# Optimization experiments

Measured on AMD Instinct MI355X. Metric: run time of the kernel, lower is better.

The kernel has to match this reference:

```python
import jax, jax.numpy as jnp
import numpy as np

LR_MEMORY = 0.01
CHUNK = 128


def _mlp(W0, b0, W1, b1, x):
    # linear -> SiLU -> linear (no activation on last layer)
    h = jax.nn.silu(x @ W0.T + b0)
    return h @ W1.T + b1


def setup_inputs() -> dict:
    key = jax.random.key(0)
    ks = jax.random.split(key, 8)
    B, L, D, M = 2, 2048, 2048, 2048
    x = jax.random.normal(ks[0], (B, L, D), jnp.float32)
    # kaiming_uniform (linear gain): bound = sqrt(3/fan_in); biases zero
    bw0 = float(np.sqrt(3.0 / D))
    bw1 = float(np.sqrt(3.0 / M))
    W0 = jax.random.uniform(ks[1], (M, D), jnp.float32, -bw0, bw0)
    b0 = jnp.zeros((M,), jnp.float32)
    W1 = jax.random.uniform(ks[2], (D, M), jnp.float32, -bw1, bw1)
    b1 = jnp.zeros((D,), jnp.float32)
    # lr_gate / forget_gate: nn.Linear(D,1) default init ~ U(-1/sqrt(D), 1/sqrt(D))
    bl = float(np.sqrt(1.0 / D))
    lr_w = jax.random.uniform(ks[3], (1, D), jnp.float32, -bl, bl)
    lr_b = jax.random.uniform(ks[4], (1,), jnp.float32, -bl, bl)
    fg_w = jax.random.uniform(ks[5], (1, D), jnp.float32, -bl, bl)
    fg_b = jax.random.uniform(ks[6], (1,), jnp.float32, -bl, bl)
    return {"x": x, "W0": W0, "b0": b0, "W1": W1, "b1": b1,
            "lr_w": lr_w, "lr_b": lr_b, "fg_w": fg_w, "fg_b": fg_b}


def reference(x, W0, b0, W1, b1, lr_w, lr_b, fg_w, fg_b):
    # Training-mode forward (create_graph=True path): gradients of the
    # chunk-wise fast-weight updates stay connected across chunks.
    B, L, D = x.shape
    C = min(CHUNK, L)
    n = L // C
    chunks = x.reshape(B, n, C, D).transpose(1, 0, 2, 3)  # (n, B, C, D)

    def loss_fn(params, chunk):
        pred = _mlp(*params, chunk)
        # target is detached in the torch code (chunk.detach())
        return jnp.mean((pred - jax.lax.stop_gradient(chunk)) ** 2)

    def step(params, chunk):
        grads = jax.grad(loss_fn)(params, chunk)
        eff_lr = LR_MEMORY * jnp.mean(jax.nn.sigmoid(chunk @ lr_w.T + lr_b))
        forget = jnp.mean(jax.nn.sigmoid(chunk.mean(axis=1) @ fg_w.T + fg_b))
        new_params = tuple(forget * p - eff_lr * g for p, g in zip(params, grads))
        out = _mlp(*new_params, chunk)  # re-forward through updated weights
        return new_params, out

    _, outs = jax.lax.scan(step, (W0, b0, W1, b1), chunks)  # outs: (n, B, C, D)
    return outs.transpose(1, 0, 2, 3).reshape(B, L, D)
```

## Files before the change

### kernel.cpp

```cpp
#include <hip/hip_runtime.h>
#include <hip/hip_bf16.h>
#include <cstddef>
#include <cstdint>

#define DD 2048
#define NRW 256
#define NCHUNK 16
#define CSZ 128
#define SCDP 4096.0f
#define NSTEP 16

typedef _Float16 h16;
typedef __attribute__((ext_vector_type(8))) _Float16 f16x8;
typedef __attribute__((ext_vector_type(4))) _Float16 f16x4;
typedef __attribute__((ext_vector_type(4))) float f32x4;

__device__ __forceinline__ float sigm(float v){ return 1.f/(1.f+__expf(-v)); }
__device__ __forceinline__ int xrow(int r, int t){ return (r>>7)*2048 + t*CSZ + (r&127); }
__device__ __forceinline__ f32x4 mfma16(f16x8 a, f16x8 b, f32x4 c){
  return __builtin_amdgcn_mfma_f32_16x16x32_f16(a, b, c, 0, 0, 0);
}

#define SBAR() do{ __builtin_amdgcn_sched_barrier(0); __builtin_amdgcn_s_barrier(); __builtin_amdgcn_sched_barrier(0); }while(0)
#define VMCNT(n) asm volatile("s_waitcnt vmcnt(" #n ")" ::: "memory")

__device__ __forceinline__ void gload16(const h16* g, h16* l){
  __builtin_amdgcn_global_load_lds((const __attribute__((address_space(1))) void*)g,
                                   (__attribute__((address_space(3))) void*)l, 16, 0, 0);
}

template<int MODE>
__global__ __launch_bounds__(512) void rowgemm(
    const h16* __restrict__ A, const h16* __restrict__ Bm,
    const float* __restrict__ bias,
    const float* __restrict__ x, int t,
    const h16* __restrict__ dsin, h16* __restrict__ dsout,
    float* __restrict__ ofp,
    h16* __restrict__ ob, h16* __restrict__ obT)
{
  __shared__ __align__(16) h16 As[3][32][128];
  __shared__ __align__(16) h16 Bs[3][64][128];
  __shared__ __align__(16) h16 Tb[64][36];
  const int tid = threadIdx.x;
  const int j0 = blockIdx.x * 64;
  const int r0 = blockIdx.y * 32;
  const int wid = tid >> 6, lane = tid & 63;
  const int wm = wid >> 2, wn = wid & 3;
  const int lr_ = lane & 15, lk = lane >> 4;
  const int sl4 = lane >> 4, su = lane & 15;
  const int arow = wid*4 + sl4;
  const int brow0 = wid*4 + sl4;
  const int brow1 = 32 + wid*4 + sl4;
  const size_t aoff  = (size_t)(r0 + arow)*DD + (size_t)((su ^ (arow&7))*8);
  const size_t boff0 = (size_t)(j0 + brow0)*DD + (size_t)((su ^ (brow0&7))*8);
  const size_t boff1 = (size_t)(j0 + brow1)*DD + (size_t)((su ^ (brow1&7))*8);
  h16* const as_base = &As[0][0][0];
  h16* const bs_base = &Bs[0][0][0];

  auto STAGE = [&](int b, int s){
    const size_t k0 = (size_t)s*128;
    gload16(A  + aoff  + k0, as_base + b*4096 + wid*512);
    gload16(Bm + boff0 + k0, bs_base + b*8192 + wid*512);
    gload16(Bm + boff1 + k0, bs_base + b*8192 + (wid+8)*512);
  };

  const int ar = wm*16 + lr_;
  const int br = wn*16 + lr_;
  int aidx[4], bidx[4];
#pragma unroll
  for (int q=0;q<4;++q){
    aidx[q] = ar*128 + ((q*4+lk)^(ar&7))*8;
    bidx[q] = br*128 + ((q*4+lk)^(br&7))*8;
  }

  f32x4 acc = {0.f,0.f,0.f,0.f};
  STAGE(0,0); STAGE(1,1);
  for (int s = 0; s < NSTEP; ++s){
    if (s < NSTEP-2){ STAGE((s+2)%3, s+2); VMCNT(6); }
    else if (s == NSTEP-2){ VMCNT(3); }
    else { VMCNT(0); }
    SBAR();
    const int cur = s%3;
    f16x8 a[4], b[4];
#pragma unroll
    for (int q=0;q<4;++q){
      a[q] = *(const f16x8*)(as_base + cur*4096 + aidx[q]);
      b[q] = *(const f16x8*)(bs_base + cur*8192 + bidx[q]);
    }
#pragma unroll
    for (int q=0;q<4;++q) acc = mfma16(a[q], b[q], acc);
    SBAR();
  }

  const int gc = j0 + wn*16 + lr_;
  const float bv = (MODE != 2) ? bias[gc] : 0.f;
#pragma unroll
  for (int ii=0;ii<4;++ii){
    const int gr = r0 + wm*16 + lk*4 + ii;
    float v = acc[ii] + bv;
    if (MODE == 0){
      float sg = sigm(v);
      float hval = v*sg;
      dsout[(size_t)gr*DD + gc] = (h16)(sg*(1.f + v*(1.f - sg)));
      ob[(size_t)gr*DD + gc] = (h16)hval;
      Tb[wn*16 + lr_][wm*16 + lk*4 + ii] = (h16)hval;
    } else if (MODE == 1){
      float xv = x[(size_t)xrow(gr,t)*DD + gc];
      float dpv = (SCDP*2.f/524288.f)*(v - xv);
      ob[(size_t)gr*DD + gc] = (h16)dpv;
      Tb[wn*16 + lr_][wm*16 + lk*4 + ii] = (h16)dpv;
    } else if (MODE == 2){
      float dzv = v * (float)dsin[(size_t)gr*DD + gc];
      Tb[wn*16 + lr_][wm*16 + lk*4 + ii] = (h16)dzv;
    } else if (MODE == 3){
      float sg = sigm(v);
      ob[(size_t)gr*DD + gc] = (h16)(v*sg);
    } else {
      ofp[(size_t)xrow(gr,t)*DD + gc] = v;
    }
  }
  if (MODE == 0 || MODE == 1 || MODE == 2){
    __syncthreads();
    const int lrow = tid >> 3, c4 = (tid & 7)*4;
    *(f16x4*)&obT[(size_t)(j0+lrow)*NRW + r0 + c4] = *(const f16x4*)&Tb[lrow][c4];
  }
}

template<int MODE>
__global__ __launch_bounds__(256) void gradup(
    const h16* __restrict__ A, const h16* __restrict__ Bm,
    h16* __restrict__ Wh, h16* __restrict__ WTh,
    const float* __restrict__ scal)
{
  __shared__ __align__(16) h16 As[2][64][128];
  __shared__ __align__(16) h16 Bs[2][64][128];
  __shared__ __align__(16) h16 Tb[64][72];
  const int tid = threadIdx.x;
  const int j0 = blockIdx.x * 64;
  const int i0 = blockIdx.y * 64;
  const int wid = tid >> 6, lane = tid & 63;
  const int wm = wid >> 1, wn = wid & 1;
  const int lr_ = lane & 15, lk = lane >> 4;
  const int sl4 = lane >> 4, su = lane & 15;
  h16* const as_base = &As[0][0][0];
  h16* const bs_base = &Bs[0][0][0];

#pragma unroll
  for (int h=0; h<2; ++h){
#pragma unroll
    for (int i=0;i<4;++i){
      const int c = wid*4 + i;
      const int row = c*4 + sl4;
      const size_t go = (size_t)row*NRW + (size_t)(h*128 + ((su ^ (row&7))*8));
      gload16(A  + (size_t)i0*NRW + go, as_base + h*8192 + c*512);
      gload16(Bm + (size_t)j0*NRW + go, bs_base + h*8192 + c*512);
    }
  }

  const int ra0 = wm*32 + lr_, ra1 = ra0 + 16;
  const int rb0 = wn*32 + lr_, rb1 = rb0 + 16;
  f32x4 acc[2][2] = {};
#pragma unroll
  for (int h=0; h<2; ++h){
    if (h==0){ VMCNT(8); } else { VMCNT(0); }
    SBAR();
#pragma unroll
    for (int ks=0; ks<4; ++ks){
      f16x8 a0 = *(const f16x8*)(as_base + h*8192 + ra0*128 + ((ks*4+lk)^(ra0&7))*8);
      f16x8 a1 = *(const f16x8*)(as_base + h*8192 + ra1*128 + ((ks*4+lk)^(ra1&7))*8);
      f16x8 b0 = *(const f16x8*)(bs_base + h*8192 + rb0*128 + ((ks*4+lk)^(rb0&7))*8);
      f16x8 b1 = *(const f16x8*)(bs_base + h*8192 + rb1*128 + ((ks*4+lk)^(rb1&7))*8);
      acc[0][0] = mfma16(a0,b0,acc[0][0]);
      acc[0][1] = mfma16(a0,b1,acc[0][1]);
      acc[1][0] = mfma16(a1,b0,acc[1][0]);
      acc[1][1] = mfma16(a1,b1,acc[1][1]);
    }
  }

  const float lrs = scal[0] * (1.f/SCDP);
  const float fg  = scal[1];
#pragma unroll
  for (int ri=0;ri<2;++ri)
#pragma unroll
  for (int cj=0;cj<2;++cj)
#pragma unroll
  for (int ii=0;ii<4;++ii){
    const int gi = i0 + wm*32 + ri*16 + lk*4 + ii;
    const int gj = j0 + wn*32 + cj*16 + lr_;
    const size_t idx = (size_t)gi*DD + gj;
    float wv = fg*(float)Wh[idx] - lrs*acc[ri][cj][ii];
    Wh[idx] = (h16)wv;
    if (MODE==0) Tb[wn*32+cj*16+lr_][wm*32+ri*16+lk*4+ii] = (h16)wv;
  }
  if (MODE==0){
    __syncthreads();
    const int lrow = tid >> 2, c16 = (tid & 3)*16;
    *(f16x8*)&WTh[(size_t)(j0+lrow)*DD + i0 + c16]   = *(const f16x8*)&Tb[lrow][c16];
    *(f16x8*)&WTh[(size_t)(j0+lrow)*DD + i0 + c16+8] = *(const f16x8*)&Tb[lrow][c16+8];
  }
}

__global__ __launch_bounds__(256) void xprep(const float* __restrict__ x, int t,
    const float* __restrict__ lr_w, const float* __restrict__ fg_w,
    h16* __restrict__ xh, h16* __restrict__ xT,
    float* __restrict__ rowacc, float* __restrict__ accs)
{
  __shared__ __align__(16) h16 Tb[64][72];
  __shared__ float red[4];
  const int tid = threadIdx.x;
  const int j0 = blockIdx.x*64, r0 = blockIdx.y*64;
  const int c4 = (tid & 15)*4, g = tid >> 4;
  const float4 lw = *(const float4*)&lr_w[j0+c4];
  const float4 fw = *(const float4*)&fg_w[j0+c4];
  float sfall = 0.f;
  float slv[4];
#pragma unroll
  for (int i=0;i<4;++i){
    const int row = g + i*16;
    float4 xv = *(const float4*)&x[(size_t)xrow(r0+row, t)*DD + j0 + c4];
    f16x4 hv; hv[0]=(h16)xv.x; hv[1]=(h16)xv.y; hv[2]=(h16)xv.z; hv[3]=(h16)xv.w;
    *(f16x4*)&xh[(size_t)(r0+row)*DD + j0 + c4] = hv;
    Tb[c4+0][row]=hv[0]; Tb[c4+1][row]=hv[1]; Tb[c4+2][row]=hv[2]; Tb[c4+3][row]=hv[3];
    float sl = xv.x*lw.x + xv.y*lw.y + xv.z*lw.z + xv.w*lw.w;
    float sf = xv.x*fw.x + xv.y*fw.y + xv.z*fw.z + xv.w*fw.w;
#pragma unroll
    for (int m=1;m<16;m<<=1) sl += __shfl_xor(sl, m);
    slv[i] = sl;
    sfall += sf;
  }
#pragma unroll
  for (int m=1;m<64;m<<=1) sfall += __shfl_xor(sfall, m);
  if ((tid&63)==0) red[tid>>6] = sfall;
  __syncthreads();
  if ((tid&15)==0){
#pragma unroll
    for (int i=0;i<4;++i) atomicAdd(&rowacc[r0 + g + i*16], slv[i]);
  }
  if (tid==0) atomicAdd(&accs[1 + (blockIdx.y>>1)], red[0]+red[1]+red[2]+red[3]);
  const int lcol = tid >> 2, r16 = (tid & 3)*16;
  *(f16x8*)&xT[(size_t)(j0+lcol)*NRW + r0 + r16]   = *(const f16x8*)&Tb[lcol][r16];
  *(f16x8*)&xT[(size_t)(j0+lcol)*NRW + r0 + r16+8] = *(const f16x8*)&Tb[lcol][r16+8];
}

__global__ __launch_bounds__(256) void finalize(
    float* __restrict__ rowacc, float* __restrict__ accs,
    const float* __restrict__ lr_b, const float* __restrict__ fg_b,
    float* __restrict__ scal)
{
  __shared__ float red[256];
  const int tid = threadIdx.x;
  float s = sigm(rowacc[tid] + lr_b[0]);
  rowacc[tid] = 0.f;
  red[tid] = s; __syncthreads();
  for (int o=128;o>0;o>>=1){ if (tid<o) red[tid]+=red[tid+o]; __syncthreads(); }
  if (tid==0){
    scal[0] = 0.01f * red[0] * (1.f/256.f);
    scal[1] = 0.5f*( sigm(accs[1]*(1.f/128.f) + fg_b[0]) + sigm(accs[2]*(1.f/128.f) + fg_b[0]) );
    accs[1] = 0.f; accs[2] = 0.f;
  }
}

__global__ __launch_bounds__(256) void bias_update(
    const h16* __restrict__ dpT, const h16* __restrict__ dzT,
    float* __restrict__ b1c, float* __restrict__ b0c,
    const float* __restrict__ scal)
{
  const int j = blockIdx.x*256 + threadIdx.x;
  const float lrs = scal[0] * (1.f/SCDP), fg = scal[1];
  const h16* src = (j < DD) ? &dpT[(size_t)j*NRW] : &dzT[(size_t)(j-DD)*NRW];
  float s = 0.f;
  const f16x8* p = (const f16x8*)src;
#pragma unroll 4
  for (int q = 0; q < 32; ++q){
    f16x8 v = p[q];
#pragma unroll
    for (int e = 0; e < 8; ++e) s += (float)v[e];
  }
  if (j < DD) b1c[j]    = fg*b1c[j]    - lrs*s;
  else        b0c[j-DD] = fg*b0c[j-DD] - lrs*s;
}

__global__ __launch_bounds__(256) void init_w1(const float* __restrict__ Wc,
    h16* __restrict__ Wh, h16* __restrict__ WTh)
{
  __shared__ __align__(16) h16 Tb[64][72];
  const int tid = threadIdx.x;
  const int j0 = blockIdx.x*64, i0 = blockIdx.y*64;
  const int c4 = (tid & 15)*4, rbase = tid >> 4;
#pragma unroll
  for (int i=0;i<4;++i){
    int row = rbase + i*16;
    float4 wv = *(const float4*)&Wc[(size_t)(i0+row)*DD + j0 + c4];
    f16x4 hv; hv[0]=(h16)wv.x; hv[1]=(h16)wv.y; hv[2]=(h16)wv.z; hv[3]=(h16)wv.w;
    *(f16x4*)&Wh[(size_t)(i0+row)*DD + j0 + c4] = hv;
    Tb[c4+0][row]=hv[0]; Tb[c4+1][row]=hv[1]; Tb[c4+2][row]=hv[2]; Tb[c4+3][row]=hv[3];
  }
  __syncthreads();
  const int lrow = tid >> 2, c16 = (tid & 3)*16;
  *(f16x8*)&WTh[(size_t)(j0+lrow)*DD + i0 + c16]   = *(const f16x8*)&Tb[lrow][c16];
  *(f16x8*)&WTh[(size_t)(j0+lrow)*DD + i0 + c16+8] = *(const f16x8*)&Tb[lrow][c16+8];
}

__global__ void init_w0(const float* __restrict__ Wc, h16* __restrict__ Wh){
  size_t i = ((size_t)blockIdx.x*256 + threadIdx.x)*4;
  float4 wv = *(const float4*)&Wc[i];
  f16x4 hv; hv[0]=(h16)wv.x; hv[1]=(h16)wv.y; hv[2]=(h16)wv.z; hv[3]=(h16)wv.w;
  *(f16x4*)&Wh[i] = hv;
}

extern "C" void kernel_launch(void* const* d_in, const int* in_sizes, int n_in,
                              void* d_out, int out_size, void* d_ws, size_t ws_size,
                              hipStream_t stream)
{
  const float* x    = (const float*)d_in[0];
  const float* W0   = (const float*)d_in[1];
  const float* b0   = (const float*)d_in[2];
  const float* W1   = (const float*)d_in[3];
  const float* b1   = (const float*)d_in[4];
  const float* lr_w = (const float*)d_in[5];
  const float* lr_b = (const float*)d_in[6];
  const float* fg_w = (const float*)d_in[7];
  const float* fg_b = (const float*)d_in[8];
  float* out = (float*)d_out;

  char* ws = (char*)d_ws;
  size_t off = 0;
  auto alloc = [&](size_t bytes)->char*{ char* p = ws + off; off += (bytes + 255) & ~255ull; return p; };
  float* b0c    = (float*)alloc(2048*4);
  float* b1c    = (float*)alloc(2048*4);
  float* stats  = (float*)alloc(1312);
  float* rowacc = stats;
  float* accs   = stats + 256;
  float* scal   = stats + 264;
  h16* W0h  = (h16*)alloc(4194304*2);
  h16* W1h  = (h16*)alloc(4194304*2);
  h16* W1Th = (h16*)alloc(4194304*2);
  h16* ds0h = (h16*)alloc(524288*2);
  h16* xh   = (h16*)alloc(524288*2);
  h16* xT   = (h16*)alloc(524288*2);
  h16* hb   = (h16*)alloc(524288*2);
  h16* hT   = (h16*)alloc(524288*2);
  h16* dpb  = (h16*)alloc(524288*2);
  h16* dpT  = (h16*)alloc(524288*2);
  h16* dzT  = (h16*)alloc(524288*2);
  h16* h2b  = (h16*)alloc(524288*2);

  hipMemcpyAsync(b0c, b0, 2048*sizeof(float), hipMemcpyDeviceToDevice, stream);
  hipMemcpyAsync(b1c, b1, 2048*sizeof(float), hipMemcpyDeviceToDevice, stream);
  hipMemsetAsync(stats, 0, 264*4, stream);

  dim3 blk256(256), blk512(512);
  init_w0<<<4096, blk256, 0, stream>>>(W0, W0h);
  init_w1<<<dim3(32,32), blk256, 0, stream>>>(W1, W1h, W1Th);

  for (int t = 0; t < NCHUNK; ++t){
    xprep<<<dim3(32,4), blk256, 0, stream>>>(x, t, lr_w, fg_w, xh, xT, rowacc, accs);
    finalize<<<1, blk256, 0, stream>>>(rowacc, accs, lr_b, fg_b, scal);
    rowgemm<0><<<dim3(32,8), blk512, 0, stream>>>(xh, W0h, b0c, nullptr, t, nullptr, ds0h, nullptr, hb, hT);
    rowgemm<1><<<dim3(32,8), blk512, 0, stream>>>(hb, W1h, b1c, x, t, nullptr, nullptr, nullptr, dpb, dpT);
    rowgemm<2><<<dim3(32,8), blk512, 0, stream>>>(dpb, W1Th, b1c, nullptr, t, ds0h, nullptr, nullptr, nullptr, dzT);
    gradup<0><<<dim3(32,32), blk256, 0, stream>>>(dpT, hT, W1h, W1Th, scal);
    gradup<1><<<dim3(32,32), blk256, 0, stream>>>(dzT, xT, W0h, nullptr, scal);
    bias_update<<<16, blk256, 0, stream>>>(dpT, dzT, b1c, b0c, scal);
    rowgemm<3><<<dim3(32,8), blk512, 0, stream>>>(xh, W0h, b0c, nullptr, t, nullptr, nullptr, nullptr, h2b, nullptr);
    rowgemm<4><<<dim3(32,8), blk512, 0, stream>>>(h2b, W1h, b1c, nullptr, t, nullptr, nullptr, out, nullptr, nullptr);
  }
}
```

Measured before the change: 1.731 ms.

## Fuse per-chunk kernel sequence into one cooperative persistent kernel with grid syncs

Replaces the roughly 160 per-chunk kernel launches with a single cooperative kernel of 256 blocks that runs all 16 chunks and separates phases with grid.sync. The x conversion and gate computation for all chunks are hoisted into two up-front batched kernels, which adds per-chunk xh/xT buffers. The weight-gradient update and bias update are merged into one phase that loops over tiles with 512 threads. The goal is to remove launch overhead and inter-kernel gaps. In exchange, each phase runs at a fixed 256-block occupancy and pays the cost of grid barriers, and the update GEMM loses its double-buffered load pipelining.

```diff
diff --git a/kernel.cpp b/kernel.cpp
--- a/kernel.cpp
+++ b/kernel.cpp
@@ -1,7 +1,10 @@
 #include <hip/hip_runtime.h>
 #include <hip/hip_bf16.h>
+#include <hip/hip_cooperative_groups.h>
 #include <cstddef>
 #include <cstdint>
+
+namespace cg = cooperative_groups;
 
 #define DD 2048
 #define NRW 256
@@ -29,33 +32,41 @@
                                    (__attribute__((address_space(3))) void*)l, 16, 0, 0);
 }
 
+union SMem {
+  struct { h16 As[3][32][128]; h16 Bs[3][64][128]; h16 Tb[64][40]; } rg;
+  struct { h16 As[64][256];    h16 Bs[64][256];    h16 Tb[64][72]; } up;
+};
+
+struct ScanArgs {
+  const h16* xh; const h16* xT;
+  h16* W0h; h16* W1h; h16* W1Th;
+  h16* ds; h16* hb; h16* hT; h16* dpb; h16* dpT; h16* dzT; h16* h2b;
+  float* b0c; float* b1c;
+  const float* x; const float* scal; float* out;
+};
+
 template<int MODE>
-__global__ __launch_bounds__(512) void rowgemm(
+__device__ void rg_phase(SMem& sm, int bid,
     const h16* __restrict__ A, const h16* __restrict__ Bm,
     const float* __restrict__ bias,
     const float* __restrict__ x, int t,
     const h16* __restrict__ dsin, h16* __restrict__ dsout,
-    float* __restrict__ ofp,
-    h16* __restrict__ ob, h16* __restrict__ obT)
-{
-  __shared__ __align__(16) h16 As[3][32][128];
-  __shared__ __align__(16) h16 Bs[3][64][128];
-  __shared__ __align__(16) h16 Tb[64][36];
+    float* __restrict__ ofp, h16* __restrict__ ob, h16* __restrict__ obT)
+{
   const int tid = threadIdx.x;
-  const int j0 = blockIdx.x * 64;
-  const int r0 = blockIdx.y * 32;
+  const int j0 = (bid & 31) * 64;
+  const int r0 = (bid >> 5) * 32;
   const int wid = tid >> 6, lane = tid & 63;
   const int wm = wid >> 2, wn = wid & 3;
   const int lr_ = lane & 15, lk = lane >> 4;
   const int sl4 = lane >> 4, su = lane & 15;
   const int arow = wid*4 + sl4;
-  const int brow0 = wid*4 + sl4;
-  const int brow1 = 32 + wid*4 + sl4;
+  const int brow1 = 32 + arow;
   const size_t aoff  = (size_t)(r0 + arow)*DD + (size_t)((su ^ (arow&7))*8);
-  const size_t boff0 = (size_t)(j0 + brow0)*DD + (size_t)((su ^ (brow0&7))*8);
+  const size_t boff0 = (size_t)(j0 + arow)*DD + (size_t)((su ^ (arow&7))*8);
   const size_t boff1 = (size_t)(j0 + brow1)*DD + (size_t)((su ^ (brow1&7))*8);
-  h16* const as_base = &As[0][0][0];
-  h16* const bs_base = &Bs[0][0][0];
+  h16* const as_base = &sm.rg.As[0][0][0];
+  h16* const bs_base = &sm.rg.Bs[0][0][0];
 
   auto STAGE = [&](int b, int s){
     const size_t k0 = (size_t)s*128;
@@ -103,15 +114,15 @@
       float hval = v*sg;
       dsout[(size_t)gr*DD + gc] = (h16)(sg*(1.f + v*(1.f - sg)));
       ob[(size_t)gr*DD + gc] = (h16)hval;
-      Tb[wn*16 + lr_][wm*16 + lk*4 + ii] = (h16)hval;
+      sm.rg.Tb[wn*16 + lr_][wm*16 + lk*4 + ii] = (h16)hval;
     } else if (MODE == 1){
       float xv = x[(size_t)xrow(gr,t)*DD + gc];
       float dpv = (SCDP*2.f/524288.f)*(v - xv);
       ob[(size_t)gr*DD + gc] = (h16)dpv;
-      Tb[wn*16 + lr_][wm*16 + lk*4 + ii] = (h16)dpv;
+      sm.rg.Tb[wn*16 + lr_][wm*16 + lk*4 + ii] = (h16)dpv;
     } else if (MODE == 2){
       float dzv = v * (float)dsin[(size_t)gr*DD + gc];
-      Tb[wn*16 + lr_][wm*16 + lk*4 + ii] = (h16)dzv;
+      sm.rg.Tb[wn*16 + lr_][wm*16 + lk*4 + ii] = (h16)dzv;
     } else if (MODE == 3){
       float sg = sigm(v);
       ob[(size_t)gr*DD + gc] = (h16)(v*sg);
@@ -122,93 +133,126 @@
   if (MODE == 0 || MODE == 1 || MODE == 2){
     __syncthreads();
     const int lrow = tid >> 3, c4 = (tid & 7)*4;
-    *(f16x4*)&obT[(size_t)(j0+lrow)*NRW + r0 + c4] = *(const f16x4*)&Tb[lrow][c4];
-  }
-}
-
-template<int MODE>
-__global__ __launch_bounds__(256) void gradup(
-    const h16* __restrict__ A, const h16* __restrict__ Bm,
-    h16* __restrict__ Wh, h16* __restrict__ WTh,
-    const float* __restrict__ scal)
-{
-  __shared__ __align__(16) h16 As[2][64][128];
-  __shared__ __align__(16) h16 Bs[2][64][128];
-  __shared__ __align__(16) h16 Tb[64][72];
+    *(f16x4*)&obT[(size_t)(j0+lrow)*NRW + r0 + c4] = *(const f16x4*)&sm.rg.Tb[lrow][c4];
+  }
+}
+
+__device__ void upd_phase(SMem& sm, int bid,
+    const h16* __restrict__ dpT, const h16* __restrict__ hT,
+    const h16* __restrict__ dzT, const h16* __restrict__ xT,
+    h16* __restrict__ W0h, h16* __restrict__ W1h, h16* __restrict__ W1Th,
+    float* __restrict__ b0c, float* __restrict__ b1c,
+    float lrs, float fg)
+{
   const int tid = threadIdx.x;
-  const int j0 = blockIdx.x * 64;
-  const int i0 = blockIdx.y * 64;
   const int wid = tid >> 6, lane = tid & 63;
-  const int wm = wid >> 1, wn = wid & 1;
+  const int wm = wid >> 2, wn = wid & 3;
   const int lr_ = lane & 15, lk = lane >> 4;
-  const int sl4 = lane >> 4, su = lane & 15;
-  h16* const as_base = &As[0][0][0];
-  h16* const bs_base = &Bs[0][0][0];
-
-#pragma unroll
-  for (int h=0; h<2; ++h){
-#pragma unroll
-    for (int i=0;i<4;++i){
-      const int c = wid*4 + i;
-      const int row = c*4 + sl4;
-      const size_t go = (size_t)row*NRW + (size_t)(h*128 + ((su ^ (row&7))*8));
-      gload16(A  + (size_t)i0*NRW + go, as_base + h*8192 + c*512);
-      gload16(Bm + (size_t)j0*NRW + go, bs_base + h*8192 + c*512);
-    }
-  }
-
-  const int ra0 = wm*32 + lr_, ra1 = ra0 + 16;
-  const int rb0 = wn*32 + lr_, rb1 = rb0 + 16;
-  f32x4 acc[2][2] = {};
-#pragma unroll
-  for (int h=0; h<2; ++h){
-    if (h==0){ VMCNT(8); } else { VMCNT(0); }
+  const int sunit = lane & 31;
+  h16* const as_base = &sm.up.As[0][0];
+  h16* const bs_base = &sm.up.Bs[0][0];
+
+  for (int it = 0; it < 8; ++it){
+    const int T = it*256 + bid;
+    const bool isW1 = (T < 1024);
+    const int TT = isW1 ? T : T - 1024;
+    const int i0 = (TT >> 5) * 64;
+    const int j0 = (TT & 31) * 64;
+    const h16* Asrc = isW1 ? dpT : dzT;
+    const h16* Bsrc = isW1 ? hT  : xT;
+#pragma unroll
+    for (int q=0; q<4; ++q){
+      const int rl = wid*8 + q*2 + (lane>>5);
+      const size_t so = (size_t)((sunit ^ (rl&7))*8);
+      gload16(Asrc + (size_t)(i0+rl)*NRW + so, as_base + (wid*8+q*2)*256);
+      gload16(Bsrc + (size_t)(j0+rl)*NRW + so, bs_base + (wid*8+q*2)*256);
+    }
+    VMCNT(0);
     SBAR();
-#pragma unroll
-    for (int ks=0; ks<4; ++ks){
-      f16x8 a0 = *(const f16x8*)(as_base + h*8192 + ra0*128 + ((ks*4+lk)^(ra0&7))*8);
-      f16x8 a1 = *(const f16x8*)(as_base + h*8192 + ra1*128 + ((ks*4+lk)^(ra1&7))*8);
-      f16x8 b0 = *(const f16x8*)(bs_base + h*8192 + rb0*128 + ((ks*4+lk)^(rb0&7))*8);
-      f16x8 b1 = *(const f16x8*)(bs_base + h*8192 + rb1*128 + ((ks*4+lk)^(rb1&7))*8);
-      acc[0][0] = mfma16(a0,b0,acc[0][0]);
-      acc[0][1] = mfma16(a0,b1,acc[0][1]);
-      acc[1][0] = mfma16(a1,b0,acc[1][0]);
-      acc[1][1] = mfma16(a1,b1,acc[1][1]);
-    }
-  }
-
-  const float lrs = scal[0] * (1.f/SCDP);
-  const float fg  = scal[1];
-#pragma unroll
-  for (int ri=0;ri<2;++ri)
-#pragma unroll
-  for (int cj=0;cj<2;++cj)
-#pragma unroll
-  for (int ii=0;ii<4;++ii){
-    const int gi = i0 + wm*32 + ri*16 + lk*4 + ii;
-    const int gj = j0 + wn*32 + cj*16 + lr_;
-    const size_t idx = (size_t)gi*DD + gj;
-    float wv = fg*(float)Wh[idx] - lrs*acc[ri][cj][ii];
-    Wh[idx] = (h16)wv;
-    if (MODE==0) Tb[wn*32+cj*16+lr_][wm*32+ri*16+lk*4+ii] = (h16)wv;
-  }
-  if (MODE==0){
+    f32x4 acc0 = {0.f,0.f,0.f,0.f}, acc1 = {0.f,0.f,0.f,0.f};
+    const int ra0 = wm*32 + lr_, ra1 = ra0 + 16, rb = wn*16 + lr_;
+#pragma unroll
+    for (int s=0; s<8; ++s){
+      const int u = s*4 + lk;
+      f16x8 b  = *(const f16x8*)(bs_base + rb*256  + ((u^(rb&7))*8));
+      f16x8 a0 = *(const f16x8*)(as_base + ra0*256 + ((u^(ra0&7))*8));
+      f16x8 a1 = *(const f16x8*)(as_base + ra1*256 + ((u^(ra1&7))*8));
+      acc0 = mfma16(a0,b,acc0);
+      acc1 = mfma16(a1,b,acc1);
+    }
+    h16* Wh = isW1 ? W1h : W0h;
+#pragma unroll
+    for (int f=0; f<2; ++f){
+      const f32x4 acc = f ? acc1 : acc0;
+      const int gi = i0 + wm*32 + f*16 + lk*4;
+      const int gj = j0 + wn*16 + lr_;
+#pragma unroll
+      for (int ii=0; ii<4; ++ii){
+        const size_t idx = (size_t)(gi+ii)*DD + gj;
+        float wv = fg*(float)Wh[idx] - lrs*acc[ii];
+        Wh[idx] = (h16)wv;
+        if (isW1) sm.up.Tb[wn*16+lr_][wm*32+f*16+lk*4+ii] = (h16)wv;
+      }
+    }
+    if (isW1){
+      __syncthreads();
+      const int lrow = tid >> 3, c8 = (tid & 7)*8;
+      *(f16x8*)&W1Th[(size_t)(j0+lrow)*DD + i0 + c8] = *(const f16x8*)&sm.up.Tb[lrow][c8];
+    }
     __syncthreads();
-    const int lrow = tid >> 2, c16 = (tid & 3)*16;
-    *(f16x8*)&WTh[(size_t)(j0+lrow)*DD + i0 + c16]   = *(const f16x8*)&Tb[lrow][c16];
-    *(f16x8*)&WTh[(size_t)(j0+lrow)*DD + i0 + c16+8] = *(const f16x8*)&Tb[lrow][c16+8];
-  }
-}
-
-__global__ __launch_bounds__(256) void xprep(const float* __restrict__ x, int t,
+  }
+  if (bid >= 248){
+    const int j = (bid-248)*512 + tid;
+    const h16* src = (j < DD) ? &dpT[(size_t)j*NRW] : &dzT[(size_t)(j-DD)*NRW];
+    float s = 0.f;
+    const f16x8* p = (const f16x8*)src;
+#pragma unroll 4
+    for (int q = 0; q < 32; ++q){
+      f16x8 v = p[q];
+#pragma unroll
+      for (int e = 0; e < 8; ++e) s += (float)v[e];
+    }
+    if (j < DD) b1c[j]    = fg*b1c[j]    - lrs*s;
+    else        b0c[j-DD] = fg*b0c[j-DD] - lrs*s;
+  }
+}
+
+__global__ __launch_bounds__(512) void scan_coop(ScanArgs a)
+{
+  __shared__ SMem sm;
+  cg::grid_group grid = cg::this_grid();
+  const int bid = blockIdx.x;
+  for (int t = 0; t < NCHUNK; ++t){
+    const h16* xh_t = a.xh + (size_t)t*524288;
+    const h16* xT_t = a.xT + (size_t)t*524288;
+    const float lrs = a.scal[2*t] * (1.f/SCDP);
+    const float fgv = a.scal[2*t+1];
+    rg_phase<0>(sm, bid, xh_t, a.W0h, a.b0c, nullptr, t, nullptr, a.ds, nullptr, a.hb, a.hT);
+    grid.sync();
+    rg_phase<1>(sm, bid, a.hb, a.W1h, a.b1c, a.x, t, nullptr, nullptr, nullptr, a.dpb, a.dpT);
+    grid.sync();
+    rg_phase<2>(sm, bid, a.dpb, a.W1Th, a.b1c, nullptr, t, a.ds, nullptr, nullptr, nullptr, a.dzT);
+    grid.sync();
+    upd_phase(sm, bid, a.dpT, a.hT, a.dzT, xT_t, a.W0h, a.W1h, a.W1Th, a.b0c, a.b1c, lrs, fgv);
+    grid.sync();
+    rg_phase<3>(sm, bid, xh_t, a.W0h, a.b0c, nullptr, t, nullptr, nullptr, nullptr, a.h2b, nullptr);
+    grid.sync();
+    rg_phase<4>(sm, bid, a.h2b, a.W1h, a.b1c, nullptr, t, nullptr, nullptr, a.out, nullptr, nullptr);
+  }
+}
+
+__global__ __launch_bounds__(256) void prepx(const float* __restrict__ x,
     const float* __restrict__ lr_w, const float* __restrict__ fg_w,
     h16* __restrict__ xh, h16* __restrict__ xT,
-    float* __restrict__ rowacc, float* __restrict__ accs)
+    float* __restrict__ rowacc, float* __restrict__ fgacc)
 {
   __shared__ __align__(16) h16 Tb[64][72];
   __shared__ float red[4];
   const int tid = threadIdx.x;
+  const int t = blockIdx.z;
   const int j0 = blockIdx.x*64, r0 = blockIdx.y*64;
+  h16* xh_t = xh + (size_t)t*524288;
+  h16* xT_t = xT + (size_t)t*524288;
   const int c4 = (tid & 15)*4, g = tid >> 4;
   const float4 lw = *(const float4*)&lr_w[j0+c4];
   const float4 fw = *(const float4*)&fg_w[j0+c4];
@@ -219,7 +263,7 @@
     const int row = g + i*16;
     float4 xv = *(const float4*)&x[(size_t)xrow(r0+row, t)*DD + j0 + c4];
     f16x4 hv; hv[0]=(h16)xv.x; hv[1]=(h16)xv.y; hv[2]=(h16)xv.z; hv[3]=(h16)xv.w;
-    *(f16x4*)&xh[(size_t)(r0+row)*DD + j0 + c4] = hv;
+    *(f16x4*)&xh_t[(size_t)(r0+row)*DD + j0 + c4] = hv;
     Tb[c4+0][row]=hv[0]; Tb[c4+1][row]=hv[1]; Tb[c4+2][row]=hv[2]; Tb[c4+3][row]=hv[3];
     float sl = xv.x*lw.x + xv.y*lw.y + xv.z*lw.z + xv.w*lw.w;
     float sf = xv.x*fw.x + xv.y*fw.y + xv.z*fw.z + xv.w*fw.w;
@@ -234,50 +278,29 @@
   __syncthreads();
   if ((tid&15)==0){
 #pragma unroll
-    for (int i=0;i<4;++i) atomicAdd(&rowacc[r0 + g + i*16], slv[i]);
-  }
-  if (tid==0) atomicAdd(&accs[1 + (blockIdx.y>>1)], red[0]+red[1]+red[2]+red[3]);
+    for (int i=0;i<4;++i) atomicAdd(&rowacc[t*256 + r0 + g + i*16], slv[i]);
+  }
+  if (tid==0) atomicAdd(&fgacc[2*t + (blockIdx.y>>1)], red[0]+red[1]+red[2]+red[3]);
   const int lcol = tid >> 2, r16 = (tid & 3)*16;
-  *(f16x8*)&xT[(size_t)(j0+lcol)*NRW + r0 + r16]   = *(const f16x8*)&Tb[lcol][r16];
-  *(f16x8*)&xT[(size_t)(j0+lcol)*NRW + r0 + r16+8] = *(const f16x8*)&Tb[lcol][r16+8];
-}
-
-__global__ __launch_bounds__(256) void finalize(
-    float* __restrict__ rowacc, float* __restrict__ accs,
+  *(f16x8*)&xT_t[(size_t)(j0+lcol)*NRW + r0 + r16]   = *(const f16x8*)&Tb[lcol][r16];
+  *(f16x8*)&xT_t[(size_t)(j0+lcol)*NRW + r0 + r16+8] = *(const f16x8*)&Tb[lcol][r16+8];
+}
+
+__global__ __launch_bounds__(256) void gates(
+    const float* __restrict__ rowacc, const float* __restrict__ fgacc,
     const float* __restrict__ lr_b, const float* __restrict__ fg_b,
     float* __restrict__ scal)
 {
   __shared__ float red[256];
-  const int tid = threadIdx.x;
-  float s = sigm(rowacc[tid] + lr_b[0]);
-  rowacc[tid] = 0.f;
-  red[tid] = s; __syncthreads();
+  const int tid = threadIdx.x, t = blockIdx.x;
+  red[tid] = sigm(rowacc[t*256+tid] + lr_b[0]);
+  __syncthreads();
   for (int o=128;o>0;o>>=1){ if (tid<o) red[tid]+=red[tid+o]; __syncthreads(); }
   if (tid==0){
-    scal[0] = 0.01f * red[0] * (1.f/256.f);
-    scal[1] = 0.5f*( sigm(accs[1]*(1.f/128.f) + fg_b[0]) + sigm(accs[2]*(1.f/128.f) + fg_b[0]) );
-    accs[1] = 0.f; accs[2] = 0.f;
-  }
-}
-
-__global__ __launch_bounds__(256) void bias_update(
-    const h16* __restrict__ dpT, const h16* __restrict__ dzT,
-    float* __restrict__ b1c, float* __restrict__ b0c,
-    const float* __restrict__ scal)
-{
-  const int j = blockIdx.x*256 + threadIdx.x;
-  const float lrs = scal[0] * (1.f/SCDP), fg = scal[1];
-  const h16* src = (j < DD) ? &dpT[(size_t)j*NRW] : &dzT[(size_t)(j-DD)*NRW];
-  float s = 0.f;
-  const f16x8* p = (const f16x8*)src;
-#pragma unroll 4
-  for (int q = 0; q < 32; ++q){
-    f16x8 v = p[q];
-#pragma unroll
-    for (int e = 0; e < 8; ++e) s += (float)v[e];
-  }
-  if (j < DD) b1c[j]    = fg*b1c[j]    - lrs*s;
-  else        b0c[j-DD] = fg*b0c[j-DD] - lrs*s;
+    scal[2*t]   = 0.01f * red[0] * (1.f/256.f);
+    scal[2*t+1] = 0.5f*( sigm(fgacc[2*t]*(1.f/128.f) + fg_b[0])
+                       + sigm(fgacc[2*t+1]*(1.f/128.f) + fg_b[0]) );
+  }
 }
 
 __global__ __launch_bounds__(256) void init_w1(const float* __restrict__ Wc,
@@ -328,16 +351,16 @@
   auto alloc = [&](size_t bytes)->char*{ char* p = ws + off; off += (bytes + 255) & ~255ull; return p; };
   float* b0c    = (float*)alloc(2048*4);
   float* b1c    = (float*)alloc(2048*4);
-  float* stats  = (float*)alloc(1312);
+  float* stats  = (float*)alloc((16*256 + 32 + 32)*4);
   float* rowacc = stats;
-  float* accs   = stats + 256;
-  float* scal   = stats + 264;
+  float* fgacc  = stats + 16*256;
+  float* scal   = stats + 16*256 + 32;
   h16* W0h  = (h16*)alloc(4194304*2);
   h16* W1h  = (h16*)alloc(4194304*2);
   h16* W1Th = (h16*)alloc(4194304*2);
-  h16* ds0h = (h16*)alloc(524288*2);
-  h16* xh   = (h16*)alloc(524288*2);
-  h16* xT   = (h16*)alloc(524288*2);
+  h16* xh   = (h16*)alloc((size_t)16*524288*2);
+  h16* xT   = (h16*)alloc((size_t)16*524288*2);
+  h16* ds   = (h16*)alloc(524288*2);
   h16* hb   = (h16*)alloc(524288*2);
   h16* hT   = (h16*)alloc(524288*2);
   h16* dpb  = (h16*)alloc(524288*2);
@@ -347,22 +370,20 @@
 
   hipMemcpyAsync(b0c, b0, 2048*sizeof(float), hipMemcpyDeviceToDevice, stream);
   hipMemcpyAsync(b1c, b1, 2048*sizeof(float), hipMemcpyDeviceToDevice, stream);
-  hipMemsetAsync(stats, 0, 264*4, stream);
-
-  dim3 blk256(256), blk512(512);
+  hipMemsetAsync(stats, 0, (16*256 + 32)*4, stream);
+
+  dim3 blk256(256);
   init_w0<<<4096, blk256, 0, stream>>>(W0, W0h);
   init_w1<<<dim3(32,32), blk256, 0, stream>>>(W1, W1h, W1Th);
-
-  for (int t = 0; t < NCHUNK; ++t){
-    xprep<<<dim3(32,4), blk256, 0, stream>>>(x, t, lr_w, fg_w, xh, xT, rowacc, accs);
-    finalize<<<1, blk256, 0, stream>>>(rowacc, accs, lr_b, fg_b, scal);
-    rowgemm<0><<<dim3(32,8), blk512, 0, stream>>>(xh, W0h, b0c, nullptr, t, nullptr, ds0h, nullptr, hb, hT);
-    rowgemm<1><<<dim3(32,8), blk512, 0, stream>>>(hb, W1h, b1c, x, t, nullptr, nullptr, nullptr, dpb, dpT);
-    rowgemm<2><<<dim3(32,8), blk512, 0, stream>>>(dpb, W1Th, b1c, nullptr, t, ds0h, nullptr, nullptr, nullptr, dzT);
-    gradup<0><<<dim3(32,32), blk256, 0, stream>>>(dpT, hT, W1h, W1Th, scal);
-    gradup<1><<<dim3(32,32), blk256, 0, stream>>>(dzT, xT, W0h, nullptr, scal);
-    bias_update<<<16, blk256, 0, stream>>>(dpT, dzT, b1c, b0c, scal);
-    rowgemm<3><<<dim3(32,8), blk512, 0, stream>>>(xh, W0h, b0c, nullptr, t, nullptr, nullptr, nullptr, h2b, nullptr);
-    rowgemm<4><<<dim3(32,8), blk512, 0, stream>>>(h2b, W1h, b1c, nullptr, t, nullptr, nullptr, out, nullptr, nullptr);
-  }
-}
+  prepx<<<dim3(32,4,16), blk256, 0, stream>>>(x, lr_w, fg_w, xh, xT, rowacc, fgacc);
+  gates<<<16, blk256, 0, stream>>>(rowacc, fgacc, lr_b, fg_b, scal);
+
+  ScanArgs sa;
+  sa.xh = xh; sa.xT = xT;
+  sa.W0h = W0h; sa.W1h = W1h; sa.W1Th = W1Th;
+  sa.ds = ds; sa.hb = hb; sa.hT = hT; sa.dpb = dpb; sa.dpT = dpT; sa.dzT = dzT; sa.h2b = h2b;
+  sa.b0c = b0c; sa.b1c = b1c;
+  sa.x = x; sa.scal = scal; sa.out = out;
+  void* kargs[] = { (void*)&sa };
+  hipLaunchCooperativeKernel((const void*)scan_coop, dim3(256), dim3(512), kargs, 0, stream);
+}
```

Result: slower. 3.949 ms (+128.1%).
